# Kernel optimization log

Measured on AMD Instinct MI355X. Metric: run time of the kernel, lower is better.

The kernel has to match this reference:

```python
import jax, jax.numpy as jnp
import numpy as np

# Grid configuration (from PointBasedTransformConfig / data dict)
G = 64                      # mast3r grid size per axis
NUM_VOXELS = G * G * G      # 262144
K = 16                      # max_points_in_voxel
RES = 0.02                  # mast3r_grid_resolution
MIN_CORNER = -(G * RES) / 2.0  # cube centered at origin, side G*RES = 1.28
N_POINTS = 2_000_000


def setup_inputs() -> dict:
    key = jax.random.key(0)
    k1, k2, k3, k4 = jax.random.split(key, 4)
    # points uniform in [-0.8, 0.8]^3 so roughly half are inside the 1.28 cube
    pts_0 = (jax.random.uniform(k1, (N_POINTS, 3), dtype=jnp.float32) - 0.5) * 1.6
    conf = jax.random.uniform(k2, (N_POINTS,), dtype=jnp.float32)
    desc = jax.random.normal(k3, (N_POINTS, 24), dtype=jnp.float32)
    desc_conf = jax.random.normal(k4, (N_POINTS,), dtype=jnp.float32)
    return {"pts_0": pts_0, "conf": conf, "desc": desc, "desc_conf": desc_conf}


def _voxelize(pts_0, conf):
    """Returns pts_in_grid: (NUM_VOXELS, K) int32 point indices (or -1)."""
    n = pts_0.shape[0]
    # voxel index per point; out-of-bounds points get sentinel id NUM_VOXELS
    idx = jnp.floor((pts_0 - MIN_CORNER) / RES).astype(jnp.int32)  # (N,3)
    valid = jnp.all((idx >= 0) & (idx < G), axis=-1)               # (N,)
    vox = idx[:, 0] * (G * G) + idx[:, 1] * G + idx[:, 2]
    vox = jnp.where(valid, vox, NUM_VOXELS)
    # stable sort by confidence, descending (jnp.argsort is stable)
    order_conf = jnp.argsort(-conf)                 # point ids, conf-desc order
    vox_c = vox[order_conf]
    # stable sort by voxel id (preserves conf-desc order within each voxel)
    order_vox = jnp.argsort(vox_c)
    vox_s = vox_c[order_vox]                        # sorted voxel ids
    pid_s = order_conf[order_vox]                   # original point ids
    # bincount + exclusive cumsum -> per-voxel offsets -> position within voxel
    counts = jnp.bincount(vox_s, length=NUM_VOXELS + 1)
    offsets = jnp.cumsum(counts) - counts
    pos = jnp.arange(n, dtype=jnp.int32) - offsets[vox_s].astype(jnp.int32)
    # capacity-bounded scatter of point ids into the voxel grid
    ok = (pos < K) & (vox_s < NUM_VOXELS)
    rows = jnp.where(ok, vox_s, NUM_VOXELS)         # dump row for rejects
    cols = jnp.where(ok, pos, 0)
    vals = jnp.where(ok, pid_s, -1).astype(jnp.int32)
    grid = jnp.full((NUM_VOXELS + 1, K), -1, dtype=jnp.int32)
    grid = grid.at[rows, cols].set(vals)
    return grid[:NUM_VOXELS]


def reference(pts_0, conf, desc, desc_conf):
    pts_in_grid = _voxelize(pts_0, conf)            # (V, K) int32
    # gather per-point features into the grid; empty slots -> 0
    feat = jnp.concatenate(
        [pts_0, conf[:, None], desc, desc_conf[:, None]], axis=-1
    )                                               # (N, 29)
    safe = jnp.maximum(pts_in_grid, 0)
    occ = (pts_in_grid >= 0)[..., None].astype(feat.dtype)
    X = feat[safe] * occ                            # (V, K, 29)
    return pts_in_grid, X
```

## Files before the change

kernel.cpp:

```cpp
#include <hip/hip_runtime.h>
#include <limits.h>
#include <math.h>

#define GRID 64
#define NUM_VOXELS (GRID * GRID * GRID)
#define KSLOTS 16
#define CAP 32
#define FEAT 29

__global__ __launch_bounds__(256) void scatter_kernel(
    const float* __restrict__ pts, const float* __restrict__ conf, int n,
    int* __restrict__ cnt, unsigned long long* __restrict__ buf) {
    int i = blockIdx.x * blockDim.x + threadIdx.x;
    if (i >= n) return;
    const float minc = (float)(-(64.0 * 0.02) / 2.0);
    const float rinv = 50.0f;
    float x = pts[(size_t)i * 3 + 0];
    float y = pts[(size_t)i * 3 + 1];
    float z = pts[(size_t)i * 3 + 2];
    int ix = (int)floorf((x - minc) * rinv);
    int iy = (int)floorf((y - minc) * rinv);
    int iz = (int)floorf((z - minc) * rinv);
    if ((unsigned)ix >= GRID || (unsigned)iy >= GRID || (unsigned)iz >= GRID) return;
    int v = ix * (GRID * GRID) + iy * GRID + iz;
    int pos = atomicAdd(&cnt[v], 1);
    if (pos < CAP) {
        unsigned int cb = __float_as_uint(conf[i]);
        unsigned long long key =
            ((unsigned long long)cb << 32) | (unsigned int)(~i);
        buf[(size_t)v * CAP + pos] = key;
    }
}

__global__ __launch_bounds__(256) void select_kernel(
    const int* __restrict__ cnt, const unsigned long long* __restrict__ buf,
    float* __restrict__ out_idx) {
    int v = blockIdx.x * blockDim.x + threadIdx.x;
    if (v >= NUM_VOXELS) return;

    unsigned long long top[KSLOTS];
    #pragma unroll
    for (int s = 0; s < KSLOTS; ++s) top[s] = 0ULL;

    int n = cnt[v];
    if (n > CAP) n = CAP;
    const unsigned long long* row = buf + (size_t)v * CAP;
    for (int j = 0; j < n; ++j) {
        unsigned long long key = row[j];
        #pragma unroll
        for (int s = 0; s < KSLOTS; ++s) {
            unsigned long long hi = key > top[s] ? key : top[s];
            unsigned long long lo = key > top[s] ? top[s] : key;
            top[s] = hi;
            key    = lo;
        }
    }
    float* o = out_idx + (size_t)v * KSLOTS;
    #pragma unroll
    for (int s = 0; s < KSLOTS; ++s) {
        unsigned long long k = top[s];
        int pid = (k != 0ULL) ? (int)(~(unsigned int)k) : -1;
        o[s] = (float)pid;
    }
}

__global__ __launch_bounds__(256) void gather_kernel(
    const float* __restrict__ pts, const float* __restrict__ conf,
    const float* __restrict__ desc, const float* __restrict__ desc_conf,
    const float* __restrict__ out_idx, float* __restrict__ out_feat) {
    const int t = threadIdx.x;
    const size_t slot0 = (size_t)blockIdx.x * 256;
    const size_t slot  = slot0 + t;

    __shared__ float st[256 * FEAT];

    int pid = (int)out_idx[slot];

    float f[FEAT];
    #pragma unroll
    for (int e = 0; e < FEAT; ++e) f[e] = 0.0f;
    if (pid >= 0) {
        f[0] = pts[(size_t)pid * 3 + 0];
        f[1] = pts[(size_t)pid * 3 + 1];
        f[2] = pts[(size_t)pid * 3 + 2];
        f[3] = conf[pid];
        const float4* d4 = (const float4*)(desc) + (size_t)pid * 6;
        #pragma unroll
        for (int q = 0; q < 6; ++q) {
            float4 d = d4[q];
            f[4 + q * 4 + 0] = d.x;
            f[4 + q * 4 + 1] = d.y;
            f[4 + q * 4 + 2] = d.z;
            f[4 + q * 4 + 3] = d.w;
        }
        f[28] = desc_conf[pid];
    }
    #pragma unroll
    for (int e = 0; e < FEAT; ++e) st[t * FEAT + e] = f[e];
    __syncthreads();

    float4* dst = (float4*)(out_feat + slot0 * FEAT);
    const float4* src = (const float4*)st;
    #pragma unroll
    for (int k = t; k < 256 * FEAT / 4; k += 256) dst[k] = src[k];
}

extern "C" void kernel_launch(void* const* d_in, const int* in_sizes, int n_in,
                              void* d_out, int out_size, void* d_ws, size_t ws_size,
                              hipStream_t stream) {
    const float* pts       = (const float*)d_in[0];
    const float* conf      = (const float*)d_in[1];
    const float* desc      = (const float*)d_in[2];
    const float* desc_conf = (const float*)d_in[3];
    const int n = in_sizes[1];

    float* out_idx  = (float*)d_out;
    float* out_feat = out_idx + (size_t)NUM_VOXELS * KSLOTS;

    int* cnt = (int*)out_feat;
    unsigned long long* buf =
        (unsigned long long*)(out_feat + NUM_VOXELS);

    hipMemsetAsync(cnt, 0, NUM_VOXELS * sizeof(int), stream);
    scatter_kernel<<<(n + 255) / 256, 256, 0, stream>>>(pts, conf, n, cnt, buf);
    select_kernel<<<NUM_VOXELS / 256, 256, 0, stream>>>(cnt, buf, out_idx);
    gather_kernel<<<(NUM_VOXELS * KSLOTS) / 256, 256, 0, stream>>>(
        pts, conf, desc, desc_conf, out_idx, out_feat);
}
```

Baseline: 251.2 us.

## Fuse top-K select into gather kernel using workspace buffers and nontemporal stores

Adds a fused select+gather kernel in which 16 threads per block compute each voxel's top-16 point ids into shared memory, and all 256 threads then gather features and write out_idx and out_feat. Per-voxel count and key buffers move into the workspace instead of aliasing the output, so select no longer has to finish before gather can overwrite that region. Output writes and desc loads use nontemporal hints. The trade-off is that only 16 of 256 threads do the serial insertion sort, which leaves most lanes idle during select, and the fused path runs only when the workspace is large enough.

Result: slower. 280.3 us (+11.6%).

```diff
diff --git a/kernel.cpp b/kernel.cpp
--- a/kernel.cpp
+++ b/kernel.cpp
@@ -7,6 +7,8 @@
 #define KSLOTS 16
 #define CAP 32
 #define FEAT 29
+
+typedef float f32x4 __attribute__((ext_vector_type(4)));
 
 __global__ __launch_bounds__(256) void scatter_kernel(
     const float* __restrict__ pts, const float* __restrict__ conf, int n,
@@ -32,16 +34,84 @@
     }
 }
 
+__global__ __launch_bounds__(256) void select_gather_kernel(
+    const float* __restrict__ pts, const float* __restrict__ conf,
+    const float* __restrict__ desc, const float* __restrict__ desc_conf,
+    const int* __restrict__ cnt, const unsigned long long* __restrict__ buf,
+    float* __restrict__ out_idx, float* __restrict__ out_feat) {
+    const int tid = threadIdx.x;
+    const int vbase = blockIdx.x * 16;
+
+    __shared__ int spid[256];
+    __shared__ __align__(16) float st[256 * FEAT];
+
+    if (tid < 16) {
+        int v = vbase + tid;
+        unsigned long long top[KSLOTS];
+        #pragma unroll
+        for (int s = 0; s < KSLOTS; ++s) top[s] = 0ULL;
+        int n = cnt[v];
+        if (n > CAP) n = CAP;
+        const unsigned long long* row = buf + (size_t)v * CAP;
+        for (int j = 0; j < n; ++j) {
+            unsigned long long key = row[j];
+            #pragma unroll
+            for (int s = 0; s < KSLOTS; ++s) {
+                unsigned long long hi = key > top[s] ? key : top[s];
+                unsigned long long lo = key > top[s] ? top[s] : key;
+                top[s] = hi;
+                key    = lo;
+            }
+        }
+        #pragma unroll
+        for (int s = 0; s < KSLOTS; ++s) {
+            unsigned long long k = top[s];
+            spid[tid * 16 + s] = (k != 0ULL) ? (int)(~(unsigned int)k) : -1;
+        }
+    }
+    __syncthreads();
+
+    int pid = spid[tid];
+    __builtin_nontemporal_store((float)pid, &out_idx[(size_t)vbase * KSLOTS + tid]);
+
+    float f[FEAT];
+    #pragma unroll
+    for (int e = 0; e < FEAT; ++e) f[e] = 0.0f;
+    if (pid >= 0) {
+        f[0] = pts[(size_t)pid * 3 + 0];
+        f[1] = pts[(size_t)pid * 3 + 1];
+        f[2] = pts[(size_t)pid * 3 + 2];
+        f[3] = conf[pid];
+        const f32x4* d4 = (const f32x4*)(desc) + (size_t)pid * 6;
+        #pragma unroll
+        for (int q = 0; q < 6; ++q) {
+            f32x4 d = __builtin_nontemporal_load(&d4[q]);
+            f[4 + q * 4 + 0] = d.x;
+            f[4 + q * 4 + 1] = d.y;
+            f[4 + q * 4 + 2] = d.z;
+            f[4 + q * 4 + 3] = d.w;
+        }
+        f[28] = desc_conf[pid];
+    }
+    #pragma unroll
+    for (int e = 0; e < FEAT; ++e) st[tid * FEAT + e] = f[e];
+    __syncthreads();
+
+    f32x4* dst = (f32x4*)(out_feat + (size_t)vbase * KSLOTS * FEAT);
+    const f32x4* src = (const f32x4*)st;
+    #pragma unroll
+    for (int k = tid; k < 256 * FEAT / 4; k += 256)
+        __builtin_nontemporal_store(src[k], &dst[k]);
+}
+
 __global__ __launch_bounds__(256) void select_kernel(
     const int* __restrict__ cnt, const unsigned long long* __restrict__ buf,
     float* __restrict__ out_idx) {
     int v = blockIdx.x * blockDim.x + threadIdx.x;
     if (v >= NUM_VOXELS) return;
-
     unsigned long long top[KSLOTS];
     #pragma unroll
     for (int s = 0; s < KSLOTS; ++s) top[s] = 0ULL;
-
     int n = cnt[v];
     if (n > CAP) n = CAP;
     const unsigned long long* row = buf + (size_t)v * CAP;
@@ -59,8 +129,7 @@
     #pragma unroll
     for (int s = 0; s < KSLOTS; ++s) {
         unsigned long long k = top[s];
-        int pid = (k != 0ULL) ? (int)(~(unsigned int)k) : -1;
-        o[s] = (float)pid;
+        o[s] = (float)((k != 0ULL) ? (int)(~(unsigned int)k) : -1);
     }
 }
 
@@ -71,11 +140,8 @@
     const int t = threadIdx.x;
     const size_t slot0 = (size_t)blockIdx.x * 256;
     const size_t slot  = slot0 + t;
-
-    __shared__ float st[256 * FEAT];
-
+    __shared__ __align__(16) float st[256 * FEAT];
     int pid = (int)out_idx[slot];
-
     float f[FEAT];
     #pragma unroll
     for (int e = 0; e < FEAT; ++e) f[e] = 0.0f;
@@ -84,23 +150,20 @@
         f[1] = pts[(size_t)pid * 3 + 1];
         f[2] = pts[(size_t)pid * 3 + 2];
         f[3] = conf[pid];
-        const float4* d4 = (const float4*)(desc) + (size_t)pid * 6;
+        const f32x4* d4 = (const f32x4*)(desc) + (size_t)pid * 6;
         #pragma unroll
         for (int q = 0; q < 6; ++q) {
-            float4 d = d4[q];
-            f[4 + q * 4 + 0] = d.x;
-            f[4 + q * 4 + 1] = d.y;
-            f[4 + q * 4 + 2] = d.z;
-            f[4 + q * 4 + 3] = d.w;
+            f32x4 d = d4[q];
+            f[4 + q * 4 + 0] = d.x; f[4 + q * 4 + 1] = d.y;
+            f[4 + q * 4 + 2] = d.z; f[4 + q * 4 + 3] = d.w;
         }
         f[28] = desc_conf[pid];
     }
     #pragma unroll
     for (int e = 0; e < FEAT; ++e) st[t * FEAT + e] = f[e];
     __syncthreads();
-
-    float4* dst = (float4*)(out_feat + slot0 * FEAT);
-    const float4* src = (const float4*)st;
+    f32x4* dst = (f32x4*)(out_feat + slot0 * FEAT);
+    const f32x4* src = (const f32x4*)st;
     #pragma unroll
     for (int k = t; k < 256 * FEAT / 4; k += 256) dst[k] = src[k];
 }
@@ -117,13 +180,23 @@
     float* out_idx  = (float*)d_out;
     float* out_feat = out_idx + (size_t)NUM_VOXELS * KSLOTS;
 
-    int* cnt = (int*)out_feat;
-    unsigned long long* buf =
-        (unsigned long long*)(out_feat + NUM_VOXELS);
-
-    hipMemsetAsync(cnt, 0, NUM_VOXELS * sizeof(int), stream);
-    scatter_kernel<<<(n + 255) / 256, 256, 0, stream>>>(pts, conf, n, cnt, buf);
-    select_kernel<<<NUM_VOXELS / 256, 256, 0, stream>>>(cnt, buf, out_idx);
-    gather_kernel<<<(NUM_VOXELS * KSLOTS) / 256, 256, 0, stream>>>(
-        pts, conf, desc, desc_conf, out_idx, out_feat);
-}
+    const size_t need = (size_t)NUM_VOXELS * 4
+                      + (size_t)NUM_VOXELS * CAP * 8;
+
+    if (ws_size >= need) {
+        int* cnt = (int*)d_ws;
+        unsigned long long* buf = (unsigned long long*)((char*)d_ws + (size_t)NUM_VOXELS * 4);
+        (void)hipMemsetAsync(cnt, 0, NUM_VOXELS * sizeof(int), stream);
+        scatter_kernel<<<(n + 255) / 256, 256, 0, stream>>>(pts, conf, n, cnt, buf);
+        select_gather_kernel<<<NUM_VOXELS / 16, 256, 0, stream>>>(
+            pts, conf, desc, desc_conf, cnt, buf, out_idx, out_feat);
+    } else {
+        int* cnt = (int*)out_feat;
+        unsigned long long* buf = (unsigned long long*)(out_feat + NUM_VOXELS);
+        (void)hipMemsetAsync(cnt, 0, NUM_VOXELS * sizeof(int), stream);
+        scatter_kernel<<<(n + 255) / 256, 256, 0, stream>>>(pts, conf, n, cnt, buf);
+        select_kernel<<<NUM_VOXELS / 256, 256, 0, stream>>>(cnt, buf, out_idx);
+        gather_kernel<<<(NUM_VOXELS * KSLOTS) / 256, 256, 0, stream>>>(
+            pts, conf, desc, desc_conf, out_idx, out_feat);
+    }
+}
```
